# Optimization experiments

Measured on AMD Instinct MI355X. Metric: run time of the kernel, lower is better.

## Reference

```python
import jax, jax.numpy as jnp
import numpy as np


def setup_inputs() -> dict:
    key = jax.random.key(0)
    k1, k2 = jax.random.split(key)
    B, H, W, D = 4096, 64, 64, 512
    inputs = jax.random.normal(k1, (B, D), dtype=jnp.float32)
    # keras 'random_uniform' initializer default range [-0.05, 0.05]
    weights_map = jax.random.uniform(k2, (H, W, D), dtype=jnp.float32,
                                     minval=-0.05, maxval=0.05)
    return {"inputs": inputs, "weights_map": weights_map}


def reference(inputs, weights_map):
    # inputs: (B, D); weights_map: (H, W, D)
    H, W, D = weights_map.shape
    flat_w = weights_map.reshape(-1, D)              # (N, D), N = H*W
    # avoids materializing the (B, N, D) difference tensor)
    x_sq = jnp.sum(inputs * inputs, axis=1, keepdims=True)    # (B, 1)
    w_sq = jnp.sum(flat_w * flat_w, axis=1)                   # (N,)
    sq_dist = x_sq - 2.0 * (inputs @ flat_w.T) + w_sq         # (B, N)
    sq_dist = jnp.maximum(sq_dist, 0.0)
    bmu_flat = jnp.argmin(sq_dist, axis=1)                    # (B,)
    bmu_y = (bmu_flat // W).astype(jnp.int32)
    bmu_x = (bmu_flat % W).astype(jnp.int32)
    bmu_indices = jnp.stack([bmu_y, bmu_x], axis=1)           # (B, 2)
    min_sq = jnp.take_along_axis(sq_dist, bmu_flat[:, None], axis=1)[:, 0]
    quantization_errors = jnp.sqrt(min_sq)                    # (B,)
    return bmu_indices, quantization_errors
```

## Files before the change

kernel.cpp:

```cpp
#include <hip/hip_runtime.h>

#define B_ROWS 4096
#define N_COLS 4096
#define DIM    512
#define LDK    1024

typedef __attribute__((ext_vector_type(8))) short short8;
typedef __attribute__((ext_vector_type(4))) float floatx4;

__device__ __forceinline__ unsigned short f2bf_rn(float f) {
    unsigned u = __float_as_uint(f);
    u += 0x7fffu + ((u >> 16) & 1u);
    return (unsigned short)(u >> 16);
}
__device__ __forceinline__ float bf2f(unsigned short h) {
    return __uint_as_float(((unsigned)h) << 16);
}

__device__ __forceinline__ unsigned long long pack_key(float v, int idx) {
    unsigned u = __float_as_uint(v);
    u = (u & 0x80000000u) ? ~u : (u | 0x80000000u);
    return ((unsigned long long)u << 32) | (unsigned)idx;
}

__device__ __forceinline__ void async16(const unsigned short* g, unsigned short* l) {
    __builtin_amdgcn_global_load_lds(
        (__attribute__((address_space(1))) void*)g,
        (__attribute__((address_space(3))) void*)l, 16, 0, 0);
}

__global__ __launch_bounds__(256) void som_convert(
    const float* __restrict__ X, const float* __restrict__ Wt,
    unsigned short* __restrict__ Xc, unsigned short* __restrict__ Wc,
    float* __restrict__ x_sq, float* __restrict__ w_sq,
    unsigned long long* __restrict__ packed)
{
    int wave = threadIdx.x >> 6, lane = threadIdx.x & 63;
    int grow = blockIdx.x * 4 + wave;
    bool isX = grow < B_ROWS;
    const float* src = isX ? (X + (size_t)grow * DIM)
                           : (Wt + (size_t)(grow - B_ROWS) * DIM);
    const float4* p4 = (const float4*)src;
    float4 a = p4[lane * 2], b = p4[lane * 2 + 1];
    float f[8] = {a.x, a.y, a.z, a.w, b.x, b.y, b.z, b.w};
    unsigned short hi[8], lo[8];
    float s = 0.f;
    #pragma unroll
    for (int t = 0; t < 8; ++t) {
        hi[t] = f2bf_rn(f[t]);
        lo[t] = f2bf_rn(f[t] - bf2f(hi[t]));
        s = fmaf(f[t], f[t], s);
    }
    unsigned short* dst = (isX ? Xc + (size_t)grow * LDK
                               : Wc + (size_t)(grow - B_ROWS) * LDK) + lane * 8;
    *(ushort4*)(dst)       = make_ushort4(hi[0], hi[1], hi[2], hi[3]);
    *(ushort4*)(dst + 4)   = make_ushort4(hi[4], hi[5], hi[6], hi[7]);
    *(ushort4*)(dst + 512) = make_ushort4(lo[0], lo[1], lo[2], lo[3]);
    *(ushort4*)(dst + 516) = make_ushort4(lo[4], lo[5], lo[6], lo[7]);
    #pragma unroll
    for (int off = 32; off >= 1; off >>= 1) s += __shfl_xor(s, off, 64);
    if (lane == 0) {
        if (isX) { x_sq[grow] = s; packed[grow] = ~0ull; }
        else     { w_sq[grow - B_ROWS] = s; }
    }
}

__global__ __launch_bounds__(256, 3) void som_dist_bf16(
    const unsigned short* __restrict__ Xc, const unsigned short* __restrict__ Wc,
    const float* __restrict__ w_sq, unsigned long long* __restrict__ packed)
{
    __shared__ unsigned short Ah[128 * 32];
    __shared__ unsigned short Al[128 * 32];
    __shared__ unsigned short Bh[128 * 32];
    __shared__ unsigned short Bl[128 * 32];
    const int tid  = threadIdx.x;
    const int wave = tid >> 6, lane = tid & 63;
    const int wr = wave >> 1, wc = wave & 1;
    const int bm = blockIdx.y, bn = blockIdx.x;
    const int quad = lane >> 4, t16 = lane & 15;

    const int srow = lane >> 2;
    const int schunk = (lane & 3) ^ ((lane >> 3) & 3);
    const int scol = schunk * 8;
    const unsigned short* gAh = Xc + (size_t)(bm * 128 + wave * 32 + srow) * LDK + scol;
    const unsigned short* gBh = Wc + (size_t)(bn * 128 + wave * 32 + srow) * LDK + scol;
    const unsigned short* gAl = gAh + 512;
    const unsigned short* gBl = gBh + 512;
    unsigned short* lAh = &Ah[(wave * 32) * 32];
    unsigned short* lAl = &Al[(wave * 32) * 32];
    unsigned short* lBh = &Bh[(wave * 32) * 32];
    unsigned short* lBl = &Bl[(wave * 32) * 32];

    const int fslot = (quad ^ ((t16 >> 1) & 3)) * 8;
    const unsigned short* pah = &Ah[(wr * 64 + t16) * 32 + fslot];
    const unsigned short* pal = &Al[(wr * 64 + t16) * 32 + fslot];
    const unsigned short* pbh = &Bh[(wc * 64 + t16) * 32 + fslot];
    const unsigned short* pbl = &Bl[(wc * 64 + t16) * 32 + fslot];

    floatx4 acc[4][4];
    #pragma unroll
    for (int i = 0; i < 4; ++i)
        #pragma unroll
        for (int j = 0; j < 4; ++j) acc[i][j] = (floatx4){0.f, 0.f, 0.f, 0.f};

    #pragma unroll 1
    for (int k0 = 0; k0 < DIM; k0 += 32) {
        __syncthreads();
        async16(gAh + k0,            lAh);
        async16(gAh + k0 + 16 * LDK, lAh + 16 * 32);
        async16(gAl + k0,            lAl);
        async16(gAl + k0 + 16 * LDK, lAl + 16 * 32);
        async16(gBh + k0,            lBh);
        async16(gBh + k0 + 16 * LDK, lBh + 16 * 32);
        async16(gBl + k0,            lBl);
        async16(gBl + k0 + 16 * LDK, lBl + 16 * 32);
        __syncthreads();

        short8 ah[4], bh[4], x[4];
        #pragma unroll
        for (int i = 0; i < 4; ++i) ah[i] = *(const short8*)(pah + i * 16 * 32);
        #pragma unroll
        for (int j = 0; j < 4; ++j) bh[j] = *(const short8*)(pbh + j * 16 * 32);
        #pragma unroll
        for (int i = 0; i < 4; ++i)
            #pragma unroll
            for (int j = 0; j < 4; ++j)
                acc[i][j] = __builtin_amdgcn_mfma_f32_16x16x32_bf16(
                    ah[i], bh[j], acc[i][j], 0, 0, 0);

        #pragma unroll
        for (int j = 0; j < 4; ++j) x[j] = *(const short8*)(pbl + j * 16 * 32);
        #pragma unroll
        for (int i = 0; i < 4; ++i)
            #pragma unroll
            for (int j = 0; j < 4; ++j)
                acc[i][j] = __builtin_amdgcn_mfma_f32_16x16x32_bf16(
                    ah[i], x[j], acc[i][j], 0, 0, 0);

        #pragma unroll
        for (int i = 0; i < 4; ++i) x[i] = *(const short8*)(pal + i * 16 * 32);
        #pragma unroll
        for (int i = 0; i < 4; ++i)
            #pragma unroll
            for (int j = 0; j < 4; ++j)
                acc[i][j] = __builtin_amdgcn_mfma_f32_16x16x32_bf16(
                    x[i], bh[j], acc[i][j], 0, 0, 0);
    }

    const int col0 = bn * 128 + wc * 64 + t16;
    float wq[4];
    #pragma unroll
    for (int j = 0; j < 4; ++j) wq[j] = w_sq[col0 + j * 16];
    const int row_base = bm * 128 + wr * 64 + quad * 4;
    #pragma unroll
    for (int i = 0; i < 4; ++i) {
        #pragma unroll
        for (int r = 0; r < 4; ++r) {
            unsigned long long best = ~0ull;
            #pragma unroll
            for (int j = 0; j < 4; ++j) {
                float val = fmaf(-2.f, acc[i][j][r], wq[j]);
                unsigned long long key = pack_key(val, col0 + j * 16);
                best = (key < best) ? key : best;
            }
            #pragma unroll
            for (int m = 1; m <= 8; m <<= 1) {
                unsigned long long o = __shfl_xor(best, m, 64);
                best = (o < best) ? o : best;
            }
            if (t16 == 0)
                atomicMin(&packed[row_base + i * 16 + r], best);
        }
    }
}

__global__ __launch_bounds__(256) void som_finalize(
    const unsigned long long* __restrict__ packed,
    const float* __restrict__ x_sq, float* __restrict__ out)
{
    int b = blockIdx.x * 256 + threadIdx.x;
    unsigned long long p = packed[b];
    unsigned idx = (unsigned)(p & 0xffffffffull);
    unsigned key = (unsigned)(p >> 32);
    unsigned u = (key & 0x80000000u) ? (key & 0x7fffffffu) : ~key;
    float val = __uint_as_float(u);
    float sq = fmaxf(x_sq[b] + val, 0.f);
    out[2 * b]     = (float)(idx >> 6);
    out[2 * b + 1] = (float)(idx & 63);
    out[2 * B_ROWS + b] = sqrtf(sq);
}

extern "C" void kernel_launch(void* const* d_in, const int* in_sizes, int n_in,
                              void* d_out, int out_size, void* d_ws, size_t ws_size,
                              hipStream_t stream) {
    const float* X  = (const float*)d_in[0];
    const float* Wt = (const float*)d_in[1];
    float* out = (float*)d_out;

    unsigned long long* packed = (unsigned long long*)d_ws;
    float* x_sq = (float*)((char*)d_ws + (32 << 10));
    float* w_sq = (float*)((char*)d_ws + (48 << 10));
    unsigned short* Xc = (unsigned short*)((char*)d_ws + (64 << 10));
    unsigned short* Wc = (unsigned short*)((char*)d_ws + (64 << 10) + ((size_t)B_ROWS * LDK * 2));

    som_convert<<<dim3((B_ROWS + N_COLS) / 4), dim3(256), 0, stream>>>(
        X, Wt, Xc, Wc, x_sq, w_sq, packed);
    som_dist_bf16<<<dim3(N_COLS / 128, B_ROWS / 128), dim3(256), 0, stream>>>(
        Xc, Wc, w_sq, packed);
    som_finalize<<<dim3(B_ROWS / 256), dim3(256), 0, stream>>>(packed, x_sq, out);
}
```

Measured before the change: 123.7 us.

## Add producer wave with double-buffered LDS and flag-based sync in distance GEMM

Adds a fifth wave that acts as a dedicated loader, streaming A/B hi/lo tiles into two LDS stages with global_load_lds. The four compute waves spin on per-stage counters in shared memory instead of using block-wide barriers, so the next k-slice can load while the current one runs through the MFMAs. This is meant to hide global load latency that the old single-buffer, two-barrier loop exposed. In exchange it doubles LDS use, caps occupancy at 2 blocks per CU, and relies on volatile spin-waits and LDS atomics for correctness, which adds polling overhead and ordering risk.

Result: slower. 146.6 us (+18.6%).

```diff
diff --git a/kernel.cpp b/kernel.cpp
--- a/kernel.cpp
+++ b/kernel.cpp
@@ -4,6 +4,7 @@
 #define N_COLS 4096
 #define DIM    512
 #define LDK    1024
+#define STAGE  16384
 
 typedef __attribute__((ext_vector_type(8))) short short8;
 typedef __attribute__((ext_vector_type(4))) float floatx4;
@@ -65,37 +66,59 @@
     }
 }
 
-__global__ __launch_bounds__(256, 3) void som_dist_bf16(
+__global__ __launch_bounds__(320, 2) void som_dist_bf16(
     const unsigned short* __restrict__ Xc, const unsigned short* __restrict__ Wc,
     const float* __restrict__ w_sq, unsigned long long* __restrict__ packed)
 {
-    __shared__ unsigned short Ah[128 * 32];
-    __shared__ unsigned short Al[128 * 32];
-    __shared__ unsigned short Bh[128 * 32];
-    __shared__ unsigned short Bl[128 * 32];
+    __shared__ unsigned short buf[2 * STAGE];
+    __shared__ unsigned syncw[4];
+    volatile unsigned* vs = syncw;
     const int tid  = threadIdx.x;
     const int wave = tid >> 6, lane = tid & 63;
-    const int wr = wave >> 1, wc = wave & 1;
     const int bm = blockIdx.y, bn = blockIdx.x;
-    const int quad = lane >> 4, t16 = lane & 15;
+
+    if (tid < 4) syncw[tid] = 0;
+    __syncthreads();
 
     const int srow = lane >> 2;
     const int schunk = (lane & 3) ^ ((lane >> 3) & 3);
     const int scol = schunk * 8;
-    const unsigned short* gAh = Xc + (size_t)(bm * 128 + wave * 32 + srow) * LDK + scol;
-    const unsigned short* gBh = Wc + (size_t)(bn * 128 + wave * 32 + srow) * LDK + scol;
-    const unsigned short* gAl = gAh + 512;
-    const unsigned short* gBl = gBh + 512;
-    unsigned short* lAh = &Ah[(wave * 32) * 32];
-    unsigned short* lAl = &Al[(wave * 32) * 32];
-    unsigned short* lBh = &Bh[(wave * 32) * 32];
-    unsigned short* lBl = &Bl[(wave * 32) * 32];
-
+
+    if (wave == 4) {
+        const unsigned short* gA = Xc + (size_t)(bm * 128 + srow) * LDK + scol;
+        const unsigned short* gB = Wc + (size_t)(bn * 128 + srow) * LDK + scol;
+        #pragma unroll 1
+        for (int g = 0; g < 16; ++g) {
+            const int s = g & 1;
+            const int k0 = g * 32;
+            if (g >= 2) {
+                const unsigned need = 4u * (unsigned)((g - s) >> 1);
+                while (vs[2 + s] < need) __builtin_amdgcn_s_sleep(1);
+            }
+            unsigned short* st = &buf[s * STAGE];
+            #pragma unroll
+            for (int rg = 0; rg < 8; ++rg)
+                async16(gA + (size_t)(rg * 16) * LDK + k0, st + rg * 16 * 32);
+            #pragma unroll
+            for (int rg = 0; rg < 8; ++rg)
+                async16(gA + (size_t)(rg * 16) * LDK + k0 + 512, st + 4096 + rg * 16 * 32);
+            #pragma unroll
+            for (int rg = 0; rg < 8; ++rg)
+                async16(gB + (size_t)(rg * 16) * LDK + k0, st + 8192 + rg * 16 * 32);
+            #pragma unroll
+            for (int rg = 0; rg < 8; ++rg)
+                async16(gB + (size_t)(rg * 16) * LDK + k0 + 512, st + 12288 + rg * 16 * 32);
+            asm volatile("s_waitcnt vmcnt(0)" ::: "memory");
+            if (lane == 0) vs[s] = (unsigned)(g + 1);
+        }
+        return;
+    }
+
+    const int wr = wave >> 1, wc = wave & 1;
+    const int quad = lane >> 4, t16 = lane & 15;
     const int fslot = (quad ^ ((t16 >> 1) & 3)) * 8;
-    const unsigned short* pah = &Ah[(wr * 64 + t16) * 32 + fslot];
-    const unsigned short* pal = &Al[(wr * 64 + t16) * 32 + fslot];
-    const unsigned short* pbh = &Bh[(wc * 64 + t16) * 32 + fslot];
-    const unsigned short* pbl = &Bl[(wc * 64 + t16) * 32 + fslot];
+    const int arow = (wr * 64 + t16) * 32 + fslot;
+    const int brow = (wc * 64 + t16) * 32 + fslot;
 
     floatx4 acc[4][4];
     #pragma unroll
@@ -104,47 +127,42 @@
         for (int j = 0; j < 4; ++j) acc[i][j] = (floatx4){0.f, 0.f, 0.f, 0.f};
 
     #pragma unroll 1
-    for (int k0 = 0; k0 < DIM; k0 += 32) {
-        __syncthreads();
-        async16(gAh + k0,            lAh);
-        async16(gAh + k0 + 16 * LDK, lAh + 16 * 32);
-        async16(gAl + k0,            lAl);
-        async16(gAl + k0 + 16 * LDK, lAl + 16 * 32);
-        async16(gBh + k0,            lBh);
-        async16(gBh + k0 + 16 * LDK, lBh + 16 * 32);
-        async16(gBl + k0,            lBl);
-        async16(gBl + k0 + 16 * LDK, lBl + 16 * 32);
-        __syncthreads();
-
-        short8 ah[4], bh[4], x[4];
-        #pragma unroll
-        for (int i = 0; i < 4; ++i) ah[i] = *(const short8*)(pah + i * 16 * 32);
-        #pragma unroll
-        for (int j = 0; j < 4; ++j) bh[j] = *(const short8*)(pbh + j * 16 * 32);
+    for (int g = 0; g < 16; ++g) {
+        const int s = g & 1;
+        while (vs[s] < (unsigned)(g + 1)) __builtin_amdgcn_s_sleep(1);
+        const unsigned short* st = &buf[s * STAGE];
+
+        short8 ah[4], al[4], bh[4], bl[4];
+        #pragma unroll
+        for (int i = 0; i < 4; ++i) ah[i] = *(const short8*)(st + arow + i * 16 * 32);
+        #pragma unroll
+        for (int i = 0; i < 4; ++i) al[i] = *(const short8*)(st + 4096 + arow + i * 16 * 32);
+        #pragma unroll
+        for (int j = 0; j < 4; ++j) bh[j] = *(const short8*)(st + 8192 + brow + j * 16 * 32);
+        #pragma unroll
+        for (int j = 0; j < 4; ++j) bl[j] = *(const short8*)(st + 12288 + brow + j * 16 * 32);
+
         #pragma unroll
         for (int i = 0; i < 4; ++i)
             #pragma unroll
             for (int j = 0; j < 4; ++j)
                 acc[i][j] = __builtin_amdgcn_mfma_f32_16x16x32_bf16(
                     ah[i], bh[j], acc[i][j], 0, 0, 0);
-
-        #pragma unroll
-        for (int j = 0; j < 4; ++j) x[j] = *(const short8*)(pbl + j * 16 * 32);
         #pragma unroll
         for (int i = 0; i < 4; ++i)
             #pragma unroll
             for (int j = 0; j < 4; ++j)
                 acc[i][j] = __builtin_amdgcn_mfma_f32_16x16x32_bf16(
-                    ah[i], x[j], acc[i][j], 0, 0, 0);
-
-        #pragma unroll
-        for (int i = 0; i < 4; ++i) x[i] = *(const short8*)(pal + i * 16 * 32);
+                    ah[i], bl[j], acc[i][j], 0, 0, 0);
         #pragma unroll
         for (int i = 0; i < 4; ++i)
             #pragma unroll
             for (int j = 0; j < 4; ++j)
                 acc[i][j] = __builtin_amdgcn_mfma_f32_16x16x32_bf16(
-                    x[i], bh[j], acc[i][j], 0, 0, 0);
+                    al[i], bh[j], acc[i][j], 0, 0, 0);
+
+        __threadfence_block();
+        if (lane == 0) atomicAdd(&syncw[2 + s], 1u);
     }
 
     const int col0 = bn * 128 + wc * 64 + t16;
@@ -205,7 +223,7 @@
 
     som_convert<<<dim3((B_ROWS + N_COLS) / 4), dim3(256), 0, stream>>>(
         X, Wt, Xc, Wc, x_sq, w_sq, packed);
-    som_dist_bf16<<<dim3(N_COLS / 128, B_ROWS / 128), dim3(256), 0, stream>>>(
+    som_dist_bf16<<<dim3(N_COLS / 128, B_ROWS / 128), dim3(320), 0, stream>>>(
         Xc, Wc, w_sq, packed);
     som_finalize<<<dim3(B_ROWS / 256), dim3(256), 0, stream>>>(packed, x_sq, out);
 }
```
